# Kernel optimization log

Hardware: AMD Instinct MI355X
Metric: run time of the kernel (lower is better)

The kernel has to match this reference:

```python
import jax, jax.numpy as jnp
import numpy as np

B, S, DM = 2, 2048, 1024
H, D = 16, 64  # num_heads, head_dim
EPS = 1e-5


def setup_inputs() -> dict:
    key = jax.random.key(0)
    ks = jax.random.split(key, 5)
    sc = 1.0 / np.sqrt(DM)
    return {
        "x": jax.random.normal(ks[0], (B, S, DM), jnp.float32),
        "wq": jax.random.normal(ks[1], (DM, DM), jnp.float32) * sc,
        "bq": jnp.zeros((DM,), jnp.float32),
        "wk": jax.random.normal(ks[2], (DM, DM), jnp.float32) * sc,
        "bk": jnp.zeros((DM,), jnp.float32),
        "wv": jax.random.normal(ks[3], (DM, DM), jnp.float32) * sc,
        "bv": jnp.zeros((DM,), jnp.float32),
        "wo": jax.random.normal(ks[4], (DM, DM), jnp.float32) * sc,
        "bo": jnp.zeros((DM,), jnp.float32),
        "alpha": jnp.ones((1,), jnp.float32),
    }


def reference(x, wq, bq, wk, bk, wv, bv, wo, bo, alpha):
    b, s, _ = x.shape
    # QKV projections -> [B, S, H, D]
    q = (x @ wq + bq).reshape(b, s, H, D)
    k = (x @ wk + bk).reshape(b, s, H, D)
    v = (x @ wv + bv).reshape(b, s, H, D)
    # YAT scores: (Q.K)^2 / (||Q-K||^2 + eps)
    dot = jnp.einsum("bqhd,bkhd->bhqk", q, k)  # [B,H,S,S]
    qn = jnp.einsum("bqhd,bqhd->bhq", q, q)    # ||q||^2
    kn = jnp.einsum("bkhd,bkhd->bhk", k, k)    # ||k||^2
    dist2 = qn[..., :, None] + kn[..., None, :] - 2.0 * dot
    scores = (dot * dot) / (dist2 + EPS)
    # alpha scaling: (sqrt(D)/log(1+D))^alpha
    scale = (jnp.sqrt(jnp.float32(D)) / jnp.log1p(jnp.float32(D))) ** alpha[0]
    attn = jax.nn.softmax(scores * scale, axis=-1)
    out = jnp.einsum("bhqk,bkhd->bqhd", attn, v).reshape(b, s, H * D)
    return out @ wo + bo
```

## Files before the change

### kernel.cpp

```cpp
#include <hip/hip_runtime.h>
#include <hip/hip_bf16.h>
#include <math.h>

typedef __bf16 bf16;
typedef bf16 bf16x4 __attribute__((ext_vector_type(4)));
typedef bf16 bf16x8 __attribute__((ext_vector_type(8)));
typedef float floatx4 __attribute__((ext_vector_type(4)));

#define MFMA16(a, b, c) __builtin_amdgcn_mfma_f32_16x16x32_bf16(a, b, c, 0, 0, 0)

__device__ __forceinline__ void split2(float v, bf16& h, bf16& l) {
    h = (bf16)v;
    l = (bf16)(v - (float)h);
}

__device__ __forceinline__ void gload16(const bf16* g, bf16* l) {
    __builtin_amdgcn_global_load_lds(
        (const __attribute__((address_space(1))) void*)g,
        (__attribute__((address_space(3))) void*)l, 16, 0, 0);
}

__global__ void split_x(const float* __restrict__ x, bf16* __restrict__ xh,
                        bf16* __restrict__ xl) {
    const int i = (blockIdx.x * 256 + threadIdx.x) * 8;
    float4 a = *(const float4*)(x + i);
    float4 b = *(const float4*)(x + i + 4);
    bf16x8 oh, ol;
    float f[8] = {a.x, a.y, a.z, a.w, b.x, b.y, b.z, b.w};
#pragma unroll
    for (int j = 0; j < 8; j++) { bf16 h, l; split2(f[j], h, l); oh[j] = h; ol[j] = l; }
    *(bf16x8*)(xh + i) = oh;
    *(bf16x8*)(xl + i) = ol;
}

__global__ void transpose_w(const float* __restrict__ wq, const float* __restrict__ wk,
                            const float* __restrict__ wv, const float* __restrict__ wo,
                            bf16* __restrict__ wt_qkv_h, bf16* __restrict__ wt_qkv_l,
                            bf16* __restrict__ wt_o_h) {
    const int z = blockIdx.z;
    const float* src = (z == 0) ? wq : (z == 1) ? wk : (z == 2) ? wv : wo;
    bf16* dsth = (z < 3) ? (wt_qkv_h + (size_t)z * 1024 * 1024) : wt_o_h;
    bf16* dstl = (z < 3) ? (wt_qkv_l + (size_t)z * 1024 * 1024) : nullptr;
    __shared__ float tile[32][33];
    const int x0 = blockIdx.x * 32, y0 = blockIdx.y * 32;
    const int tx = threadIdx.x, ty = threadIdx.y;
    for (int i = 0; i < 32; i += 8)
        tile[ty + i][tx] = src[(size_t)(y0 + ty + i) * 1024 + x0 + tx];
    __syncthreads();
    for (int i = 0; i < 32; i += 8) {
        bf16 h, l;
        split2(tile[tx][ty + i], h, l);
        dsth[(size_t)(x0 + ty + i) * 1024 + y0 + tx] = h;
        if (dstl) dstl[(size_t)(x0 + ty + i) * 1024 + y0 + tx] = l;
    }
}

__global__ __launch_bounds__(256, 2) void gemm_qkv3(
    const bf16* __restrict__ Ah, const bf16* __restrict__ Al,
    const bf16* __restrict__ Bth, const bf16* __restrict__ Btl,
    const float* __restrict__ bq, const float* __restrict__ bk,
    const float* __restrict__ bv,
    bf16* __restrict__ Qh, bf16* __restrict__ Ql,
    bf16* __restrict__ Kh, bf16* __restrict__ Kl, bf16* __restrict__ VtG) {
    __shared__ bf16 Ash[128 * 32];
    __shared__ bf16 Asl[128 * 32];
    __shared__ bf16 Bsh[128 * 32];
    __shared__ bf16 Bsl[128 * 32];

    const int t = threadIdx.x;
    const int lane = t & 63, wave = t >> 6;
    const int quad = lane >> 4, l16 = lane & 15;
    const int m0 = blockIdx.x * 128, n0 = blockIdx.y * 128;
    const int wm = (wave >> 1) * 64, wn = (wave & 1) * 64;
    const bool full = (n0 < 2048);

    const int srow = wave * 16 + (lane >> 2);
    const int scol = (lane & 3) * 8;
    const bf16* gAh = Ah + (size_t)(m0 + srow) * 1024 + scol;
    const bf16* gAl = Al + (size_t)(m0 + srow) * 1024 + scol;
    const bf16* gBh = Bth + (size_t)(n0 + srow) * 1024 + scol;
    const bf16* gBl = Btl + (size_t)(n0 + srow) * 1024 + scol;
    bf16* lAh = &Ash[wave * 16 * 32];
    bf16* lAl = &Asl[wave * 16 * 32];
    bf16* lBh = &Bsh[wave * 16 * 32];
    bf16* lBl = &Bsl[wave * 16 * 32];

    floatx4 acc[4][4] = {};

    for (int k0 = 0; k0 < 1024; k0 += 32) {
        gload16(gAh + k0, lAh);
        gload16(gAh + 64 * 1024 + k0, lAh + 64 * 32);
        gload16(gBh + k0, lBh);
        gload16(gBh + 64 * 1024 + k0, lBh + 64 * 32);
        if (full) {
            gload16(gAl + k0, lAl);
            gload16(gAl + 64 * 1024 + k0, lAl + 64 * 32);
            gload16(gBl + k0, lBl);
            gload16(gBl + 64 * 1024 + k0, lBl + 64 * 32);
        }
        __syncthreads();
        bf16x8 afh[4], bfh[4];
#pragma unroll
        for (int i = 0; i < 4; i++)
            afh[i] = *(bf16x8*)&Ash[(wm + i * 16 + l16) * 32 + quad * 8];
#pragma unroll
        for (int j = 0; j < 4; j++)
            bfh[j] = *(bf16x8*)&Bsh[(wn + j * 16 + l16) * 32 + quad * 8];
        if (full) {
            bf16x8 afl[4], bfl[4];
#pragma unroll
            for (int i = 0; i < 4; i++)
                afl[i] = *(bf16x8*)&Asl[(wm + i * 16 + l16) * 32 + quad * 8];
#pragma unroll
            for (int j = 0; j < 4; j++)
                bfl[j] = *(bf16x8*)&Bsl[(wn + j * 16 + l16) * 32 + quad * 8];
#pragma unroll
            for (int i = 0; i < 4; i++)
#pragma unroll
                for (int j = 0; j < 4; j++) {
                    acc[i][j] = MFMA16(afh[i], bfh[j], acc[i][j]);
                    acc[i][j] = MFMA16(afh[i], bfl[j], acc[i][j]);
                    acc[i][j] = MFMA16(afl[i], bfh[j], acc[i][j]);
                }
        } else {
#pragma unroll
            for (int i = 0; i < 4; i++)
#pragma unroll
                for (int j = 0; j < 4; j++)
                    acc[i][j] = MFMA16(afh[i], bfh[j], acc[i][j]);
        }
        __syncthreads();
    }

    const int which = n0 >> 10;
    const float* bias = (which == 0) ? bq : (which == 1) ? bk : bv;
#pragma unroll
    for (int i = 0; i < 4; i++)
#pragma unroll
        for (int j = 0; j < 4; j++) {
            const int col = n0 + wn + j * 16 + l16;
            const int o = col & 1023;
            const int h = o >> 6, d = o & 63;
            const float bvv = bias[o];
            const int gm0 = m0 + wm + i * 16 + quad * 4;
            const int b = gm0 >> 11;
            if (which == 2) {
                bf16x4 pv;
#pragma unroll
                for (int r = 0; r < 4; r++) pv[r] = (bf16)(acc[i][j][r] + bvv);
                const int s0 = gm0 & 2047;
                *(bf16x4*)&VtG[((size_t)((b * 16 + h) * 64 + d)) * 2048 + s0] = pv;
            } else {
#pragma unroll
                for (int r = 0; r < 4; r++) {
                    const int gm = gm0 + r;
                    const int s = gm & 2047;
                    const size_t idx = (size_t)((b * 16 + h) * 2048 + s) * 64 + d;
                    const float val = acc[i][j][r] + bvv;
                    bf16 hi, lo;
                    split2(val, hi, lo);
                    if (which == 0) { Qh[idx] = hi; Ql[idx] = lo; }
                    else            { Kh[idx] = hi; Kl[idx] = lo; }
                }
            }
        }
}

__global__ void kn_kernel(const bf16* __restrict__ Kh, const bf16* __restrict__ Kl,
                          float* __restrict__ knG) {
    const int i = blockIdx.x * 256 + threadIdx.x;
    const bf16* ph = Kh + (size_t)i * 64;
    const bf16* pl = Kl + (size_t)i * 64;
    float s = 0.f;
#pragma unroll
    for (int d0 = 0; d0 < 64; d0 += 8) {
        bf16x8 vh = *(const bf16x8*)(ph + d0);
        bf16x8 vl = *(const bf16x8*)(pl + d0);
#pragma unroll
        for (int j = 0; j < 8; j++) { float x = (float)vh[j] + (float)vl[j]; s += x * x; }
    }
    knG[i] = s;
}

__global__ __launch_bounds__(256, 2) void attn_kernel(
    const bf16* __restrict__ Qh, const bf16* __restrict__ Ql,
    const bf16* __restrict__ Kh, const bf16* __restrict__ Kl,
    const bf16* __restrict__ VtG, const float* __restrict__ knG,
    bf16* __restrict__ O, const float* __restrict__ alphap) {
    __shared__ bf16 Ksh[2][64 * 72];
    __shared__ bf16 Ksl[2][64 * 72];
    __shared__ bf16 Vs[2][64 * 72];
    __shared__ bf16 Pt[4][32 * 72];
    __shared__ float knL[2][64];

    const int t = threadIdx.x, lane = t & 63, wave = t >> 6;
    const int quad = lane >> 4, l16 = lane & 15;
    const int bh = blockIdx.x;
    const int qw = blockIdx.y * 128 + wave * 32;

    const float alpha = alphap[0];
    const float C = powf(8.0f / log1pf(64.0f), alpha) * 1.44269504f;

    const size_t qrow0 = ((size_t)bh * 2048 + qw + l16) * 64;
    const size_t qrow1 = qrow0 + 16 * 64;
    bf16x8 bq0h[2], bq1h[2], bq0l[2], bq1l[2];
    bq0h[0] = *(const bf16x8*)(Qh + qrow0 + quad * 8);
    bq1h[0] = *(const bf16x8*)(Qh + qrow0 + 32 + quad * 8);
    bq0l[0] = *(const bf16x8*)(Ql + qrow0 + quad * 8);
    bq1l[0] = *(const bf16x8*)(Ql + qrow0 + 32 + quad * 8);
    bq0h[1] = *(const bf16x8*)(Qh + qrow1 + quad * 8);
    bq1h[1] = *(const bf16x8*)(Qh + qrow1 + 32 + quad * 8);
    bq0l[1] = *(const bf16x8*)(Ql + qrow1 + quad * 8);
    bq1l[1] = *(const bf16x8*)(Ql + qrow1 + 32 + quad * 8);

    float qne[2];
#pragma unroll
    for (int qg = 0; qg < 2; qg++) {
        float qn = 0.f;
#pragma unroll
        for (int j = 0; j < 8; j++) {
            float x0 = (float)bq0h[qg][j] + (float)bq0l[qg][j];
            float x1 = (float)bq1h[qg][j] + (float)bq1l[qg][j];
            qn += x0 * x0 + x1 * x1;
        }
        qn += __shfl_xor(qn, 16, 64);
        qn += __shfl_xor(qn, 32, 64);
        qne[qg] = qn + 1e-5f;
    }

    floatx4 acco[2][4] = {};
    float m_i[2] = {0.f, 0.f};
    float l_i[2] = {0.f, 0.f};

    const int srow = t >> 3;
    const int scol = (t & 7) * 8;
    const size_t vrow0 = ((size_t)bh * 64 + srow) * 2048;
    const size_t vrow1 = ((size_t)bh * 64 + srow + 32) * 2048;
    const float* knB = knG + (size_t)bh * 2048;

    auto do_chunk = [&](int ib) {
        const bf16* KshC = Ksh[ib];
        const bf16* KslC = Ksl[ib];
        const bf16* VsC = Vs[ib];
        const float* knC = knL[ib];
        float pbuf[2][4][4];
        float mloc[2] = {0.f, 0.f};
#pragma unroll
        for (int sub = 0; sub < 4; sub++) {
            bf16x8 a0h = *(bf16x8*)&KshC[(sub * 16 + l16) * 72 + quad * 8];
            bf16x8 a1h = *(bf16x8*)&KshC[(sub * 16 + l16) * 72 + 32 + quad * 8];
            bf16x8 a0l = *(bf16x8*)&KslC[(sub * 16 + l16) * 72 + quad * 8];
            bf16x8 a1l = *(bf16x8*)&KslC[(sub * 16 + l16) * 72 + 32 + quad * 8];
            floatx4 ac0 = {}, ac1 = {};
            ac0 = MFMA16(a0h, bq0h[0], ac0);
            ac0 = MFMA16(a1h, bq1h[0], ac0);
            ac0 = MFMA16(a0h, bq0l[0], ac0);
            ac0 = MFMA16(a1h, bq1l[0], ac0);
            ac0 = MFMA16(a0l, bq0h[0], ac0);
            ac0 = MFMA16(a1l, bq1h[0], ac0);
            ac1 = MFMA16(a0h, bq0h[1], ac1);
            ac1 = MFMA16(a1h, bq1h[1], ac1);
            ac1 = MFMA16(a0h, bq0l[1], ac1);
            ac1 = MFMA16(a1h, bq1l[1], ac1);
            ac1 = MFMA16(a0l, bq0h[1], ac1);
            ac1 = MFMA16(a1l, bq1h[1], ac1);
            const floatx4 knv = *(const floatx4*)&knC[sub * 16 + quad * 4];
#pragma unroll
            for (int r = 0; r < 4; r++) {
                const float d0 = ac0[r];
                const float d1 = ac1[r];
                const float e0 = fmaf(-2.0f, d0, qne[0] + knv[r]);
                const float e1 = fmaf(-2.0f, d1, qne[1] + knv[r]);
                const float s0 = C * d0 * d0 * __builtin_amdgcn_rcpf(e0);
                const float s1 = C * d1 * d1 * __builtin_amdgcn_rcpf(e1);
                pbuf[0][sub][r] = s0;
                pbuf[1][sub][r] = s1;
                mloc[0] = fmaxf(mloc[0], s0);
                mloc[1] = fmaxf(mloc[1], s1);
            }
        }
        bf16* Pw = Pt[wave];
#pragma unroll
        for (int qg = 0; qg < 2; qg++) {
            float mx = mloc[qg];
            mx = fmaxf(mx, __shfl_xor(mx, 16, 64));
            mx = fmaxf(mx, __shfl_xor(mx, 32, 64));
            const float mnew = fmaxf(m_i[qg], mx);
            const float al = __builtin_amdgcn_exp2f(m_i[qg] - mnew);
            float rs = 0.f;
            bf16* Pq = Pw + (qg * 16 + l16) * 72;
#pragma unroll
            for (int sub = 0; sub < 4; sub++) {
                bf16x4 pv;
#pragma unroll
                for (int r = 0; r < 4; r++) {
                    const float p = __builtin_amdgcn_exp2f(pbuf[qg][sub][r] - mnew);
                    rs += p;
                    pv[r] = (bf16)p;
                }
                *(bf16x4*)&Pq[sub * 16 + quad * 4] = pv;
            }
            rs += __shfl_xor(rs, 16, 64);
            rs += __shfl_xor(rs, 32, 64);
            l_i[qg] = l_i[qg] * al + rs;
            m_i[qg] = mnew;
#pragma unroll
            for (int dsub = 0; dsub < 4; dsub++) acco[qg][dsub] *= al;
        }
        bf16x8 bp0[2], bp1[2];
#pragma unroll
        for (int qg = 0; qg < 2; qg++) {
            bp0[qg] = *(bf16x8*)&Pw[(qg * 16 + l16) * 72 + quad * 8];
            bp1[qg] = *(bf16x8*)&Pw[(qg * 16 + l16) * 72 + 32 + quad * 8];
        }
#pragma unroll
        for (int dsub = 0; dsub < 4; dsub++) {
            bf16x8 a0 = *(bf16x8*)&VsC[(dsub * 16 + l16) * 72 + quad * 8];
            bf16x8 a1 = *(bf16x8*)&VsC[(dsub * 16 + l16) * 72 + 32 + quad * 8];
            acco[0][dsub] = MFMA16(a0, bp0[0], acco[0][dsub]);
            acco[0][dsub] = MFMA16(a1, bp1[0], acco[0][dsub]);
            acco[1][dsub] = MFMA16(a0, bp0[1], acco[1][dsub]);
            acco[1][dsub] = MFMA16(a1, bp1[1], acco[1][dsub]);
        }
    };

    {
        const size_t kb = (size_t)(bh * 2048) * 64;
        bf16x8 k0 = *(const bf16x8*)(Kh + kb + srow * 64 + scol);
        bf16x8 k1 = *(const bf16x8*)(Kh + kb + (32 + srow) * 64 + scol);
        bf16x8 c0 = *(const bf16x8*)(Kl + kb + srow * 64 + scol);
        bf16x8 c1 = *(const bf16x8*)(Kl + kb + (32 + srow) * 64 + scol);
        bf16x8 v0 = *(const bf16x8*)(VtG + vrow0 + scol);
        bf16x8 v1 = *(const bf16x8*)(VtG + vrow1 + scol);
        *(bf16x8*)&Ksh[0][srow * 72 + scol] = k0;
        *(bf16x8*)&Ksh[0][(32 + srow) * 72 + scol] = k1;
        *(bf16x8*)&Ksl[0][srow * 72 + scol] = c0;
        *(bf16x8*)&Ksl[0][(32 + srow) * 72 + scol] = c1;
        *(bf16x8*)&Vs[0][srow * 72 + scol] = v0;
        *(bf16x8*)&Vs[0][(32 + srow) * 72 + scol] = v1;
        if (t < 16) *(float4*)&knL[0][t * 4] = *(const float4*)(knB + t * 4);
    }
    __syncthreads();

    for (int ic = 0; ic < 31; ic++) {
        const int cur = ic & 1, nxt = cur ^ 1;
        const int kc = (ic + 1) * 64;
        const size_t kb = (size_t)(bh * 2048 + kc) * 64;
        bf16x8 nk0 = *(const bf16x8*)(Kh + kb + srow * 64 + scol);
        bf16x8 nk1 = *(const bf16x8*)(Kh + kb + (32 + srow) * 64 + scol);
        bf16x8 nc0 = *(const bf16x8*)(Kl + kb + srow * 64 + scol);
        bf16x8 nc1 = *(const bf16x8*)(Kl + kb + (32 + srow) * 64 + scol);
        bf16x8 nv0 = *(const bf16x8*)(VtG + vrow0 + kc + scol);
        bf16x8 nv1 = *(const bf16x8*)(VtG + vrow1 + kc + scol);
        float4 nkn;
        if (t < 16) nkn = *(const float4*)(knB + kc + t * 4);

        do_chunk(cur);

        *(bf16x8*)&Ksh[nxt][srow * 72 + scol] = nk0;
        *(bf16x8*)&Ksh[nxt][(32 + srow) * 72 + scol] = nk1;
        *(bf16x8*)&Ksl[nxt][srow * 72 + scol] = nc0;
        *(bf16x8*)&Ksl[nxt][(32 + srow) * 72 + scol] = nc1;
        *(bf16x8*)&Vs[nxt][srow * 72 + scol] = nv0;
        *(bf16x8*)&Vs[nxt][(32 + srow) * 72 + scol] = nv1;
        if (t < 16) *(float4*)&knL[nxt][t * 4] = nkn;
        __syncthreads();
    }
    do_chunk(1);

    const int b = bh >> 4, h = bh & 15;
#pragma unroll
    for (int qg = 0; qg < 2; qg++) {
        const int s = qw + qg * 16 + l16;
        const float rl = 1.0f / l_i[qg];
        const size_t obase = (size_t)(b * 2048 + s) * 1024 + h * 64;
#pragma unroll
        for (int dsub = 0; dsub < 4; dsub++) {
            bf16x4 ov;
#pragma unroll
            for (int r = 0; r < 4; r++) ov[r] = (bf16)(acco[qg][dsub][r] * rl);
            *(bf16x4*)&O[obase + dsub * 16 + quad * 4] = ov;
        }
    }
}

__global__ __launch_bounds__(256, 2) void gemm_out(
    const bf16* __restrict__ A, const bf16* __restrict__ Bt,
    const float* __restrict__ bias, float* __restrict__ outC) {
    __shared__ bf16 As[128 * 32];
    __shared__ bf16 Bs[128 * 32];

    const int t = threadIdx.x;
    const int lane = t & 63, wave = t >> 6;
    const int quad = lane >> 4, l16 = lane & 15;
    const int m0 = blockIdx.x * 128, n0 = blockIdx.y * 128;
    const int wm = (wave >> 1) * 64, wn = (wave & 1) * 64;

    const int srow = wave * 16 + (lane >> 2);
    const int scol = (lane & 3) * 8;
    const bf16* gA0 = A + (size_t)(m0 + srow) * 1024 + scol;
    const bf16* gB0 = Bt + (size_t)(n0 + srow) * 1024 + scol;
    bf16* lA = &As[wave * 16 * 32];
    bf16* lB = &Bs[wave * 16 * 32];

    floatx4 acc[4][4] = {};

    for (int k0 = 0; k0 < 1024; k0 += 32) {
        gload16(gA0 + k0, lA);
        gload16(gA0 + 64 * 1024 + k0, lA + 64 * 32);
        gload16(gB0 + k0, lB);
        gload16(gB0 + 64 * 1024 + k0, lB + 64 * 32);
        __syncthreads();
        bf16x8 af[4], bf_[4];
#pragma unroll
        for (int i = 0; i < 4; i++)
            af[i] = *(bf16x8*)&As[(wm + i * 16 + l16) * 32 + quad * 8];
#pragma unroll
        for (int j = 0; j < 4; j++)
            bf_[j] = *(bf16x8*)&Bs[(wn + j * 16 + l16) * 32 + quad * 8];
#pragma unroll
        for (int i = 0; i < 4; i++)
#pragma unroll
            for (int j = 0; j < 4; j++)
                acc[i][j] = MFMA16(af[i], bf_[j], acc[i][j]);
        __syncthreads();
    }

#pragma unroll
    for (int i = 0; i < 4; i++)
#pragma unroll
        for (int j = 0; j < 4; j++) {
            const int col = n0 + wn + j * 16 + l16;
            const float bvv = bias[col];
#pragma unroll
            for (int r = 0; r < 4; r++) {
                const int gm = m0 + wm + i * 16 + quad * 4 + r;
                outC[(size_t)gm * 1024 + col] = acc[i][j][r] + bvv;
            }
        }
}

extern "C" void kernel_launch(void* const* d_in, const int* in_sizes, int n_in,
                              void* d_out, int out_size, void* d_ws, size_t ws_size,
                              hipStream_t stream) {
    const float* x  = (const float*)d_in[0];
    const float* wq = (const float*)d_in[1];
    const float* bq = (const float*)d_in[2];
    const float* wk = (const float*)d_in[3];
    const float* bk = (const float*)d_in[4];
    const float* wv = (const float*)d_in[5];
    const float* bv = (const float*)d_in[6];
    const float* wo = (const float*)d_in[7];
    const float* bo = (const float*)d_in[8];
    const float* alpha = (const float*)d_in[9];

    char* ws = (char*)d_ws;
    const size_t MB = 1024 * 1024;
    bf16* wqkv_h = (bf16*)(ws);
    bf16* wqkv_l = (bf16*)(ws + 6 * MB);
    bf16* wo_h   = (bf16*)(ws + 12 * MB);
    float* knG   = (float*)(ws + 14 * MB);
    bf16* x_h    = (bf16*)(ws + 16 * MB);
    bf16* x_l    = (bf16*)(ws + 24 * MB);
    bf16* Q_h    = (bf16*)(ws + 32 * MB);
    bf16* Q_l    = (bf16*)(ws + 40 * MB);
    bf16* K_h    = (bf16*)(ws + 48 * MB);
    bf16* K_l    = (bf16*)(ws + 56 * MB);
    bf16* Vt_g   = (bf16*)(ws + 64 * MB);
    bf16* Ob     = (bf16*)(ws);

    split_x<<<dim3(2048), 256, 0, stream>>>(x, x_h, x_l);
    transpose_w<<<dim3(32, 32, 4), dim3(32, 8), 0, stream>>>(
        wq, wk, wv, wo, wqkv_h, wqkv_l, wo_h);
    gemm_qkv3<<<dim3(32, 24), 256, 0, stream>>>(
        x_h, x_l, wqkv_h, wqkv_l, bq, bk, bv, Q_h, Q_l, K_h, K_l, Vt_g);
    kn_kernel<<<dim3(256), 256, 0, stream>>>(K_h, K_l, knG);
    attn_kernel<<<dim3(32, 16), 256, 0, stream>>>(
        Q_h, Q_l, K_h, K_l, Vt_g, knG, Ob, alpha);
    gemm_out<<<dim3(32, 8), 256, 0, stream>>>(Ob, wo_h, bo, (float*)d_out);
}
```

Baseline: 293.1 us.

## Use 32x32 MFMA in QKV GEMM and fuse x split into weight transpose

Switches the QKV projection GEMM from 16x16x32 to 32x32x16 bf16 MFMA tiles, which reduces LDS fragment reads per MFMA and uses the larger matrix instruction. The epilogue is rewritten to match the 32x32 accumulator layout. The x hi/lo split kernel is also merged into the weight transpose kernel as an extra grid slice, saving one launch. Risk lies in accumulator layout correctness and the higher register pressure from 16-wide accumulators.

```diff
diff --git a/kernel.cpp b/kernel.cpp
--- a/kernel.cpp
+++ b/kernel.cpp
@@ -6,8 +6,10 @@
 typedef bf16 bf16x4 __attribute__((ext_vector_type(4)));
 typedef bf16 bf16x8 __attribute__((ext_vector_type(8)));
 typedef float floatx4 __attribute__((ext_vector_type(4)));
+typedef float floatx16 __attribute__((ext_vector_type(16)));
 
 #define MFMA16(a, b, c) __builtin_amdgcn_mfma_f32_16x16x32_bf16(a, b, c, 0, 0, 0)
+#define MFMA32(a, b, c) __builtin_amdgcn_mfma_f32_32x32x16_bf16(a, b, c, 0, 0, 0)
 
 __device__ __forceinline__ void split2(float v, bf16& h, bf16& l) {
     h = (bf16)v;
@@ -20,24 +22,30 @@
         (__attribute__((address_space(3))) void*)l, 16, 0, 0);
 }
 
-__global__ void split_x(const float* __restrict__ x, bf16* __restrict__ xh,
-                        bf16* __restrict__ xl) {
-    const int i = (blockIdx.x * 256 + threadIdx.x) * 8;
-    float4 a = *(const float4*)(x + i);
-    float4 b = *(const float4*)(x + i + 4);
-    bf16x8 oh, ol;
-    float f[8] = {a.x, a.y, a.z, a.w, b.x, b.y, b.z, b.w};
-#pragma unroll
-    for (int j = 0; j < 8; j++) { bf16 h, l; split2(f[j], h, l); oh[j] = h; ol[j] = l; }
-    *(bf16x8*)(xh + i) = oh;
-    *(bf16x8*)(xl + i) = ol;
-}
-
-__global__ void transpose_w(const float* __restrict__ wq, const float* __restrict__ wk,
+__global__ void prep_kernel(const float* __restrict__ xf,
+                            const float* __restrict__ wq, const float* __restrict__ wk,
                             const float* __restrict__ wv, const float* __restrict__ wo,
+                            bf16* __restrict__ xh, bf16* __restrict__ xl,
                             bf16* __restrict__ wt_qkv_h, bf16* __restrict__ wt_qkv_l,
                             bf16* __restrict__ wt_o_h) {
     const int z = blockIdx.z;
+    if (z == 4) {
+        const int tid = threadIdx.y * 32 + threadIdx.x;
+        const int bid = blockIdx.y * 32 + blockIdx.x;
+        const size_t i = ((size_t)bid * 256 + tid) * 16;
+#pragma unroll
+        for (int half = 0; half < 2; half++) {
+            float4 a = *(const float4*)(xf + i + half * 8);
+            float4 b = *(const float4*)(xf + i + half * 8 + 4);
+            bf16x8 oh, ol;
+            float f[8] = {a.x, a.y, a.z, a.w, b.x, b.y, b.z, b.w};
+#pragma unroll
+            for (int j = 0; j < 8; j++) { bf16 h, l; split2(f[j], h, l); oh[j] = h; ol[j] = l; }
+            *(bf16x8*)(xh + i + half * 8) = oh;
+            *(bf16x8*)(xl + i + half * 8) = ol;
+        }
+        return;
+    }
     const float* src = (z == 0) ? wq : (z == 1) ? wk : (z == 2) ? wv : wo;
     bf16* dsth = (z < 3) ? (wt_qkv_h + (size_t)z * 1024 * 1024) : wt_o_h;
     bf16* dstl = (z < 3) ? (wt_qkv_l + (size_t)z * 1024 * 1024) : nullptr;
@@ -69,7 +77,7 @@
 
     const int t = threadIdx.x;
     const int lane = t & 63, wave = t >> 6;
-    const int quad = lane >> 4, l16 = lane & 15;
+    const int l31 = lane & 31, hh = lane >> 5;
     const int m0 = blockIdx.x * 128, n0 = blockIdx.y * 128;
     const int wm = (wave >> 1) * 64, wn = (wave & 1) * 64;
     const bool full = (n0 < 2048);
@@ -85,7 +93,7 @@
     bf16* lBh = &Bsh[wave * 16 * 32];
     bf16* lBl = &Bsl[wave * 16 * 32];
 
-    floatx4 acc[4][4] = {};
+    floatx16 acc[2][2] = {};
 
     for (int k0 = 0; k0 < 1024; k0 += 32) {
         gload16(gAh + k0, lAh);
@@ -99,35 +107,47 @@
             gload16(gBl + 64 * 1024 + k0, lBl + 64 * 32);
         }
         __syncthreads();
-        bf16x8 afh[4], bfh[4];
-#pragma unroll
-        for (int i = 0; i < 4; i++)
-            afh[i] = *(bf16x8*)&Ash[(wm + i * 16 + l16) * 32 + quad * 8];
-#pragma unroll
-        for (int j = 0; j < 4; j++)
-            bfh[j] = *(bf16x8*)&Bsh[(wn + j * 16 + l16) * 32 + quad * 8];
+        bf16x8 Afh[2][2], Bfh[2][2];
+#pragma unroll
+        for (int ti = 0; ti < 2; ti++)
+#pragma unroll
+            for (int s = 0; s < 2; s++)
+                Afh[ti][s] = *(bf16x8*)&Ash[(wm + ti * 32 + l31) * 32 + s * 16 + hh * 8];
+#pragma unroll
+        for (int tj = 0; tj < 2; tj++)
+#pragma unroll
+            for (int s = 0; s < 2; s++)
+                Bfh[tj][s] = *(bf16x8*)&Bsh[(wn + tj * 32 + l31) * 32 + s * 16 + hh * 8];
         if (full) {
-            bf16x8 afl[4], bfl[4];
-#pragma unroll
-            for (int i = 0; i < 4; i++)
-                afl[i] = *(bf16x8*)&Asl[(wm + i * 16 + l16) * 32 + quad * 8];
-#pragma unroll
-            for (int j = 0; j < 4; j++)
-                bfl[j] = *(bf16x8*)&Bsl[(wn + j * 16 + l16) * 32 + quad * 8];
-#pragma unroll
-            for (int i = 0; i < 4; i++)
-#pragma unroll
-                for (int j = 0; j < 4; j++) {
-                    acc[i][j] = MFMA16(afh[i], bfh[j], acc[i][j]);
-                    acc[i][j] = MFMA16(afh[i], bfl[j], acc[i][j]);
-                    acc[i][j] = MFMA16(afl[i], bfh[j], acc[i][j]);
-                }
+            bf16x8 Afl[2][2], Bfl[2][2];
+#pragma unroll
+            for (int ti = 0; ti < 2; ti++)
+#pragma unroll
+                for (int s = 0; s < 2; s++)
+                    Afl[ti][s] = *(bf16x8*)&Asl[(wm + ti * 32 + l31) * 32 + s * 16 + hh * 8];
+#pragma unroll
+            for (int tj = 0; tj < 2; tj++)
+#pragma unroll
+                for (int s = 0; s < 2; s++)
+                    Bfl[tj][s] = *(bf16x8*)&Bsl[(wn + tj * 32 + l31) * 32 + s * 16 + hh * 8];
+#pragma unroll
+            for (int ti = 0; ti < 2; ti++)
+#pragma unroll
+                for (int tj = 0; tj < 2; tj++)
+#pragma unroll
+                    for (int s = 0; s < 2; s++) {
+                        acc[ti][tj] = MFMA32(Afh[ti][s], Bfh[tj][s], acc[ti][tj]);
+                        acc[ti][tj] = MFMA32(Afh[ti][s], Bfl[tj][s], acc[ti][tj]);
+                        acc[ti][tj] = MFMA32(Afl[ti][s], Bfh[tj][s], acc[ti][tj]);
+                    }
         } else {
 #pragma unroll
-            for (int i = 0; i < 4; i++)
-#pragma unroll
-                for (int j = 0; j < 4; j++)
-                    acc[i][j] = MFMA16(afh[i], bfh[j], acc[i][j]);
+            for (int ti = 0; ti < 2; ti++)
+#pragma unroll
+                for (int tj = 0; tj < 2; tj++)
+#pragma unroll
+                    for (int s = 0; s < 2; s++)
+                        acc[ti][tj] = MFMA32(Afh[ti][s], Bfh[tj][s], acc[ti][tj]);
         }
         __syncthreads();
     }
@@ -135,32 +155,35 @@
     const int which = n0 >> 10;
     const float* bias = (which == 0) ? bq : (which == 1) ? bk : bv;
 #pragma unroll
-    for (int i = 0; i < 4; i++)
-#pragma unroll
-        for (int j = 0; j < 4; j++) {
-            const int col = n0 + wn + j * 16 + l16;
+    for (int ti = 0; ti < 2; ti++)
+#pragma unroll
+        for (int tj = 0; tj < 2; tj++) {
+            const int col = n0 + wn + tj * 32 + l31;
             const int o = col & 1023;
-            const int h = o >> 6, d = o & 63;
+            const int hd = o >> 6, d = o & 63;
             const float bvv = bias[o];
-            const int gm0 = m0 + wm + i * 16 + quad * 4;
-            const int b = gm0 >> 11;
-            if (which == 2) {
-                bf16x4 pv;
-#pragma unroll
-                for (int r = 0; r < 4; r++) pv[r] = (bf16)(acc[i][j][r] + bvv);
-                const int s0 = gm0 & 2047;
-                *(bf16x4*)&VtG[((size_t)((b * 16 + h) * 64 + d)) * 2048 + s0] = pv;
-            } else {
-#pragma unroll
-                for (int r = 0; r < 4; r++) {
-                    const int gm = gm0 + r;
-                    const int s = gm & 2047;
-                    const size_t idx = (size_t)((b * 16 + h) * 2048 + s) * 64 + d;
-                    const float val = acc[i][j][r] + bvv;
-                    bf16 hi, lo;
-                    split2(val, hi, lo);
-                    if (which == 0) { Qh[idx] = hi; Ql[idx] = lo; }
-                    else            { Kh[idx] = hi; Kl[idx] = lo; }
+#pragma unroll
+            for (int g = 0; g < 4; g++) {
+                const int gm0 = m0 + wm + ti * 32 + 8 * g + 4 * hh;
+                const int b = gm0 >> 11;
+                if (which == 2) {
+                    bf16x4 pv;
+#pragma unroll
+                    for (int r = 0; r < 4; r++) pv[r] = (bf16)(acc[ti][tj][4 * g + r] + bvv);
+                    const int s0 = gm0 & 2047;
+                    *(bf16x4*)&VtG[((size_t)((b * 16 + hd) * 64 + d)) * 2048 + s0] = pv;
+                } else {
+#pragma unroll
+                    for (int r = 0; r < 4; r++) {
+                        const int gm = gm0 + r;
+                        const int s = gm & 2047;
+                        const size_t idx = (size_t)((b * 16 + hd) * 2048 + s) * 64 + d;
+                        const float val = acc[ti][tj][4 * g + r] + bvv;
+                        bf16 hi, lo;
+                        split2(val, hi, lo);
+                        if (which == 0) { Qh[idx] = hi; Ql[idx] = lo; }
+                        else            { Kh[idx] = hi; Kl[idx] = lo; }
+                    }
                 }
             }
         }
@@ -469,9 +492,8 @@
     bf16* Vt_g   = (bf16*)(ws + 64 * MB);
     bf16* Ob     = (bf16*)(ws);
 
-    split_x<<<dim3(2048), 256, 0, stream>>>(x, x_h, x_l);
-    transpose_w<<<dim3(32, 32, 4), dim3(32, 8), 0, stream>>>(
-        wq, wk, wv, wo, wqkv_h, wqkv_l, wo_h);
+    prep_kernel<<<dim3(32, 32, 5), dim3(32, 8), 0, stream>>>(
+        x, wq, wk, wv, wo, x_h, x_l, wqkv_h, wqkv_l, wo_h);
     gemm_qkv3<<<dim3(32, 24), 256, 0, stream>>>(
         x_h, x_l, wqkv_h, wqkv_l, bq, bk, bv, Q_h, Q_l, K_h, K_l, Vt_g);
     kn_kernel<<<dim3(256), 256, 0, stream>>>(K_h, K_l, knG);
```

After: 303.8 us. 1.04x slower.
